# Kernel optimization log

Hardware: AMD Instinct MI355X
Metric: run time of the kernel (lower is better)

Reference implementation:

```python
import jax, jax.numpy as jnp
import numpy as np

K = 1.0      # Lorentz curvature param (geoopt convention: <x,x>_L = -K)
SQK = 1.0    # sqrt(K)
B, LOOKBACK, SEG, D = 256, 4096, 32, 256
N = LOOKBACK // SEG  # 128 segments


def _mink_inner(x, y):
    # Minkowski inner product, keepdims on last axis
    return -x[..., :1] * y[..., :1] + jnp.sum(x[..., 1:] * y[..., 1:], axis=-1, keepdims=True)


def _expmap0_spatial(v):
    # v: [..., D] spatial tangent at origin -> point on hyperboloid [..., D+1]
    n = jnp.linalg.norm(v, axis=-1, keepdims=True)
    ns = jnp.maximum(n, 1e-9)
    x0 = SQK * jnp.cosh(n / SQK)
    xr = SQK * jnp.sinh(n / SQK) * v / ns
    return jnp.concatenate([x0, xr], axis=-1)


def _projx(x):
    # re-project onto hyperboloid: x0 = sqrt(K + ||x_spatial||^2)
    xr = x[..., 1:]
    x0 = jnp.sqrt(K + jnp.sum(xr * xr, axis=-1, keepdims=True))
    return jnp.concatenate([x0, xr], axis=-1)


def _origin_like(x):
    return jnp.zeros_like(x).at[..., 0].set(SQK)


def _logmap(x, y):
    # log_x(y) on the Lorentz manifold
    alpha = jnp.maximum(-_mink_inner(x, y) / K, 1.0 + 1e-7)
    dist = SQK * jnp.arccosh(alpha)
    u = y - alpha * x  # tangent direction (unnormalized)
    un = jnp.sqrt(jnp.maximum(_mink_inner(u, u), 1e-12))
    return dist * u / un


def _expmap(x, u):
    # exp_x(u) on the Lorentz manifold
    un = jnp.sqrt(jnp.maximum(_mink_inner(u, u), 1e-12))
    theta = un / SQK
    return jnp.cosh(theta) * x + jnp.sinh(theta) * SQK * u / un


def _clip_norm(v, max_norm):
    # euclidean-norm clip (torch.norm semantics in source)
    n = jnp.linalg.norm(v, axis=-1, keepdims=True)
    return v / jnp.maximum(n, 1e-12) * jnp.minimum(n, max_norm)


def _encode(x, W, b):
    # [B, lookback] -> [B, N, D]; dropout is identity at eval
    xs = x.reshape(B, N, SEG)
    return jnp.einsum('bns,ds->bnd', xs, W) + b


def _to_hyperbolic(z, effective_scale):
    # vectorized over all segments (original looped over seg_idx)
    v = z * jnp.tanh(effective_scale)
    n = jnp.maximum(jnp.linalg.norm(v, axis=-1, keepdims=True), 1e-8)
    v = v / n * jnp.minimum(n, 1.5)
    return _projx(_expmap0_spatial(v))


def _lorentz_fusion(pts, w):
    # pts: [4, B, N, D+1], w: [4] softmax weights; weighted Karcher mean
    o = _origin_like(pts[0])
    t0 = _logmap(o, pts)                       # tangents at origin (time comp == 0)
    wt = _clip_norm(jnp.einsum('c,cbnd->bnd', w, t0), 2.0)
    mean = _projx(_expmap0_spatial(wt[..., 1:]))  # geoopt expmap0 uses spatial part
    for _ in range(5):                         # fixed 5 Karcher iterations
        tv = _logmap(mean, pts)                # [4, B, N, D+1]
        wv = _clip_norm(jnp.einsum('c,cbnd->bnd', w, tv), 2.0)
        mean = _projx(_expmap(mean, 0.1 * wv))
    return mean


def setup_inputs() -> dict:
    key = jax.random.key(0)
    ks = jax.random.split(key, 12)
    wscale = 1.0 / np.sqrt(SEG)
    inp = {
        'trend': jax.random.normal(ks[0], (B, LOOKBACK), jnp.float32),
        'seasonal_coarse': jax.random.normal(ks[1], (B, LOOKBACK), jnp.float32),
        'seasonal_fine': jax.random.normal(ks[2], (B, LOOKBACK), jnp.float32),
        'residual': jax.random.normal(ks[3], (B, LOOKBACK), jnp.float32),
        'W_trend': jax.random.normal(ks[4], (D, SEG), jnp.float32) * wscale,
        'b_trend': jnp.zeros((D,), jnp.float32),
        'W_coarse': jax.random.normal(ks[5], (D, SEG), jnp.float32) * wscale,
        'b_coarse': jnp.zeros((D,), jnp.float32),
        'W_fine': jax.random.normal(ks[6], (D, SEG), jnp.float32) * wscale,
        'b_fine': jnp.zeros((D,), jnp.float32),
        'W_residual': jax.random.normal(ks[7], (D, SEG), jnp.float32) * wscale,
        'b_residual': jnp.zeros((D,), jnp.float32),
        'effective_scale': jnp.asarray(0.001, jnp.float32),
        'lorentz_weights': jnp.ones((4,), jnp.float32) * 0.25,
    }
    return inp


def reference(trend, seasonal_coarse, seasonal_fine, residual,
              W_trend, b_trend, W_coarse, b_coarse, W_fine, b_fine,
              W_residual, b_residual, effective_scale, lorentz_weights):
    z_t = _encode(trend, W_trend, b_trend)
    z_c = _encode(seasonal_coarse, W_coarse, b_coarse)
    z_f = _encode(seasonal_fine, W_fine, b_fine)
    z_r = _encode(residual, W_residual, b_residual)
    h_t = _to_hyperbolic(z_t, effective_scale)
    h_c = _to_hyperbolic(z_c, effective_scale)
    h_f = _to_hyperbolic(z_f, effective_scale)
    h_r = _to_hyperbolic(z_r, effective_scale)
    w = jax.nn.softmax(lorentz_weights)
    combined = _lorentz_fusion(jnp.stack([h_t, h_c, h_f, h_r], axis=0), w)
    return (h_t, h_c, h_f, h_r, combined)
```

## Files before the change

kernel.cpp:

```cpp
#include <hip/hip_runtime.h>
#include <math.h>

namespace {

typedef float f4 __attribute__((ext_vector_type(4)));

constexpr int PPW  = 4;
constexpr int WPB  = 4;
constexpr int PPB  = PPW * WPB;
constexpr int NPTS = 256 * 128;
constexpr int GRID = NPTS / PPB;
constexpr int OUTS = 257;
constexpr size_t HOFF = (size_t)NPTS * OUTS;
constexpr int LSTR = 256;

__device__ __forceinline__ float frcp(float x)   { return __builtin_amdgcn_rcpf(x); }
__device__ __forceinline__ float fsqrt_(float x) { return __builtin_amdgcn_sqrtf(x); }
__device__ __forceinline__ float facosh(float a) {
  return __logf(a + fsqrt_(fmaf(a, a, -1.f)));
}
__device__ __forceinline__ void fsinhcosh(float x, float& sh, float& ch) {
  float e = __expf(x), ei = frcp(e);
  sh = 0.5f * (e - ei);
  ch = 0.5f * (e + ei);
}
__device__ __forceinline__ float fsinh(float x) {
  float e = __expf(x);
  return 0.5f * (e - frcp(e));
}
__device__ __forceinline__ float dot4(f4 a, f4 b) {
  return a.x * b.x + a.y * b.y + a.z * b.z + a.w * b.w;
}
__device__ __forceinline__ f4 fma4s(float a, f4 b, f4 c) {
  f4 av = {a, a, a, a};
  return __builtin_elementwise_fma(av, b, c);
}

template <int CTRL>
__device__ __forceinline__ float dpp_add(float x) {
  int t = __builtin_amdgcn_update_dpp(0, __builtin_bit_cast(int, x), CTRL, 0xf, 0xf, true);
  return x + __builtin_bit_cast(float, t);
}

template <int NB>
__device__ __forceinline__ void grp_reduce(float* v) {
#pragma unroll
  for (int i = 0; i < NB; ++i) {
    float t = v[i];
    t = dpp_add<0x128>(t);
    t = dpp_add<0x124>(t);
    t = dpp_add<0x122>(t);
    t = dpp_add<0x121>(t);
    v[i] = t;
  }
}

__global__ __launch_bounds__(256) void splmw_kernel(
    const float* __restrict__ xt, const float* __restrict__ xc,
    const float* __restrict__ xf, const float* __restrict__ xr,
    const float* __restrict__ Wt, const float* __restrict__ bt,
    const float* __restrict__ Wc, const float* __restrict__ bc,
    const float* __restrict__ Wf, const float* __restrict__ bf,
    const float* __restrict__ Wr, const float* __restrict__ br,
    const float* __restrict__ esp, const float* __restrict__ lwp,
    float* __restrict__ out) {
  __shared__ float wlds[32 * LSTR];

  const int tid  = threadIdx.x;
  const int lane = tid & 63;
  const int m    = lane & 15;
  const int grp  = lane >> 4;
  const int wv   = tid >> 6;
  const int pt   = blockIdx.x * PPB + wv * PPW + grp;

  float es2 = __expf(2.f * esp[0]);
  const float ts = (es2 - 1.f) * frcp(es2 + 1.f);
  float l0 = lwp[0], l1 = lwp[1], l2 = lwp[2], l3 = lwp[3];
  float mx = fmaxf(fmaxf(l0, l1), fmaxf(l2, l3));
  float e0 = __expf(l0 - mx), e1 = __expf(l1 - mx);
  float e2 = __expf(l2 - mx), e3 = __expf(l3 - mx);
  float ei = frcp(e0 + e1 + e2 + e3);
  const float wgt[4] = {e0 * ei, e1 * ei, e2 * ei, e3 * ei};

  const float* xsarr[4] = {xt, xc, xf, xr};
  const float* Wsarr[4] = {Wt, Wc, Wf, Wr};
  const float* Bsarr[4] = {bt, bc, bf, br};

  f4    h[4][4];
  float x0s[4];
  float r2s[4];

#pragma unroll
  for (int c = 0; c < 4; ++c) {
    const float* Wp = Wsarr[c];
    f4 wrow[8];
#pragma unroll
    for (int k = 0; k < 8; ++k) wrow[k] = *(const f4*)(Wp + tid * 32 + 4 * k);
    __syncthreads();
#pragma unroll
    for (int k = 0; k < 8; ++k) {
      wlds[(4 * k + 0) * LSTR + tid] = wrow[k].x;
      wlds[(4 * k + 1) * LSTR + tid] = wrow[k].y;
      wlds[(4 * k + 2) * LSTR + tid] = wrow[k].z;
      wlds[(4 * k + 3) * LSTR + tid] = wrow[k].w;
    }
    __syncthreads();

    f4 acc[4];
    const float* bp = Bsarr[c];
#pragma unroll
    for (int j = 0; j < 4; ++j) acc[j] = *(const f4*)(bp + 4 * m + 64 * j);
    const float* xp = xsarr[c] + (size_t)pt * 32;
#pragma unroll
    for (int s4 = 0; s4 < 8; ++s4) {
      f4 xq = *(const f4*)(xp + 4 * s4);
      float xa[4] = {xq.x, xq.y, xq.z, xq.w};
#pragma unroll
      for (int si = 0; si < 4; ++si) {
        const float* wr = &wlds[(4 * s4 + si) * LSTR + 4 * m];
#pragma unroll
        for (int j = 0; j < 4; ++j)
          acc[j] = fma4s(xa[si], *(const f4*)(wr + 64 * j), acc[j]);
      }
    }

    float pa = 0.f;
#pragma unroll
    for (int j = 0; j < 4; ++j) {
      h[c][j] = ts * acc[j];
      pa += dot4(h[c][j], h[c][j]);
    }
    grp_reduce<1>(&pa);
    {
      float n1  = fsqrt_(pa);
      float n1m = fmaxf(n1, 1e-8f);
      float c1  = fminf(n1m, 1.5f) * frcp(n1m);
      float n2  = c1 * n1;
      float nsx = fmaxf(n2, 1e-9f);
      float sh  = fsinh(n2);
      float rn  = frcp(nsx);
      float g   = sh * c1 * rn;
      float sxr = sh * n2 * rn;
      float xx0 = fsqrt_(fmaf(sxr, sxr, 1.f));
#pragma unroll
      for (int j = 0; j < 4; ++j) h[c][j] = g * h[c][j];
      x0s[c] = xx0;
      r2s[c] = g * g * pa;
      float* o = out + (size_t)c * HOFF + (size_t)pt * OUTS;
      if (m == 0) o[0] = xx0;
#pragma unroll
      for (int j = 0; j < 4; ++j) {
        int base = 1 + 4 * m + 64 * j;
        f4 v = h[c][j];
        o[base] = v.x; o[base + 1] = v.y; o[base + 2] = v.z; o[base + 3] = v.w;
      }
    }
  }

  float wt0 = 0.f;
  f4    wtr[4];
#pragma unroll
  for (int j = 0; j < 4; ++j) wtr[j] = (f4){0.f, 0.f, 0.f, 0.f};
#pragma unroll
  for (int c = 0; c < 4; ++c) {
    float y0    = x0s[c];
    float alpha = fmaxf(y0, 1.f + 1e-7f);
    float dist  = facosh(alpha);
    float u0    = y0 - alpha;
    float msq   = r2s[c] - u0 * u0;
    float un    = fsqrt_(fmaxf(msq, 1e-12f));
    float f     = wgt[c] * dist * frcp(un);
    wt0 = fmaf(f, u0, wt0);
#pragma unroll
    for (int j = 0; j < 4; ++j) wtr[j] = fma4s(f, h[c][j], wtr[j]);
  }
  float rrp = 0.f;
#pragma unroll
  for (int j = 0; j < 4; ++j) rrp += dot4(wtr[j], wtr[j]);
  grp_reduce<1>(&rrp);

  f4    mr[4];
  float mrr, m0;
  {
    float rr  = rrp;
    float nrm = fsqrt_(fmaf(wt0, wt0, rr));
    float scl = fminf(nrm, 2.f) * frcp(fmaxf(nrm, 1e-12f));
    float nr  = scl * fsqrt_(rr);
    float nsx = fmaxf(nr, 1e-9f);
    float g   = fsinh(nr) * scl * frcp(nsx);
#pragma unroll
    for (int j = 0; j < 4; ++j) mr[j] = g * wtr[j];
    mrr = g * g * rr;
    m0  = fsqrt_(1.f + mrr);
  }

#pragma unroll 1
  for (int it = 0; it < 5; ++it) {
    float dots[4];
#pragma unroll
    for (int c = 0; c < 4; ++c) {
      float d = 0.f;
#pragma unroll
      for (int j = 0; j < 4; ++j) d += dot4(mr[j], h[c][j]);
      dots[c] = d;
    }
    grp_reduce<4>(dots);

    float wv0 = 0.f;
    f4    wvr[4];
#pragma unroll
    for (int j = 0; j < 4; ++j) wvr[j] = (f4){0.f, 0.f, 0.f, 0.f};
#pragma unroll
    for (int c = 0; c < 4; ++c) {
      float d     = dots[c];
      float y0    = x0s[c];
      float ip    = fmaf(m0, y0, -d);
      float alpha = fmaxf(ip, 1.f + 1e-7f);
      float dist  = facosh(alpha);
      float u0    = fmaf(-alpha, m0, y0);
      float t   = fmaf(alpha, mrr, -2.f * d);
      float s2  = fmaf(alpha, t, r2s[c]);
      float msq = s2 - u0 * u0;
      float un  = fsqrt_(fmaxf(msq, 1e-12f));
      float f   = wgt[c] * dist * frcp(un);
      wv0 = fmaf(f, u0, wv0);
#pragma unroll
      for (int j = 0; j < 4; ++j) {
        f4 diff = fma4s(-alpha, mr[j], h[c][j]);
        wvr[j]  = fma4s(f, diff, wvr[j]);
      }
    }
    float pr[2] = {0.f, 0.f};
#pragma unroll
    for (int j = 0; j < 4; ++j) {
      pr[0] += dot4(wvr[j], wvr[j]);
      pr[1] += dot4(mr[j], wvr[j]);
    }
    grp_reduce<2>(pr);

    {
      float rr2  = pr[0];
      float mwv  = pr[1];
      float nrm2 = fsqrt_(fmaf(wv0, wv0, rr2));
      float sc2  = fminf(nrm2, 2.f) * frcp(fmaxf(nrm2, 1e-12f));
      float tt   = 0.1f * sc2;
      float msqu = tt * tt * (rr2 - wv0 * wv0);
      float un2  = fsqrt_(fmaxf(msqu, 1e-12f));
      float shv, chv;
      fsinhcosh(un2, shv, chv);
      float gg = shv * tt * frcp(un2);
#pragma unroll
      for (int j = 0; j < 4; ++j) mr[j] = fma4s(chv, mr[j], gg * wvr[j]);
      mrr = chv * chv * mrr + 2.f * chv * gg * mwv + gg * gg * rr2;
      m0  = fsqrt_(1.f + mrr);
    }
  }

  {
    float* o = out + 4 * HOFF + (size_t)pt * OUTS;
    if (m == 0) o[0] = m0;
#pragma unroll
    for (int j = 0; j < 4; ++j) {
      int base = 1 + 4 * m + 64 * j;
      f4 v = mr[j];
      o[base] = v.x; o[base + 1] = v.y; o[base + 2] = v.z; o[base + 3] = v.w;
    }
  }
}

}

extern "C" void kernel_launch(void* const* d_in, const int* in_sizes, int n_in,
                              void* d_out, int out_size, void* d_ws, size_t ws_size,
                              hipStream_t stream) {
  (void)in_sizes; (void)n_in; (void)out_size; (void)d_ws; (void)ws_size;
  splmw_kernel<<<GRID, 256, 0, stream>>>(
      (const float*)d_in[0], (const float*)d_in[1], (const float*)d_in[2],
      (const float*)d_in[3], (const float*)d_in[4], (const float*)d_in[5],
      (const float*)d_in[6], (const float*)d_in[7], (const float*)d_in[8],
      (const float*)d_in[9], (const float*)d_in[10], (const float*)d_in[11],
      (const float*)d_in[12], (const float*)d_in[13], (float*)d_out);
}
```

Baseline: 281.3 us.

## Reorganize encoder GEMV so each lane computes four points, transpose via LDS

The encoder matmul is restructured so each lane owns four output columns across all four points of its wave. Each weight f4 read from LDS is then reused for four points instead of one, which cuts LDS read traffic. The accumulators are written to a per-wave LDS scratch buffer (padded stride) and read back in the original per-group layout for the rest of the pipeline. This adds an LDS round trip, more LDS allocation, and relies on a wave barrier for intra-wave ordering.

```diff
diff --git a/kernel.cpp b/kernel.cpp
--- a/kernel.cpp
+++ b/kernel.cpp
@@ -12,7 +12,8 @@
 constexpr int GRID = NPTS / PPB;
 constexpr int OUTS = 257;
 constexpr size_t HOFF = (size_t)NPTS * OUTS;
-constexpr int LSTR = 256;
+constexpr int WSTR = 256;
+constexpr int HSTR = 260;
 
 __device__ __forceinline__ float frcp(float x)   { return __builtin_amdgcn_rcpf(x); }
 __device__ __forceinline__ float fsqrt_(float x) { return __builtin_amdgcn_sqrtf(x); }
@@ -64,14 +65,17 @@
     const float* __restrict__ Wr, const float* __restrict__ br,
     const float* __restrict__ esp, const float* __restrict__ lwp,
     float* __restrict__ out) {
-  __shared__ float wlds[32 * LSTR];
+  __shared__ float wlds[32 * WSTR];
+  __shared__ float hlds[WPB * PPW * HSTR];
 
   const int tid  = threadIdx.x;
   const int lane = tid & 63;
   const int m    = lane & 15;
   const int grp  = lane >> 4;
-  const int wv   = tid >> 6;
-  const int pt   = blockIdx.x * PPB + wv * PPW + grp;
+  const int wv   = __builtin_amdgcn_readfirstlane(tid >> 6);
+  const int pt0  = blockIdx.x * PPB + wv * PPW;
+  const int pt   = pt0 + grp;
+  float* hw = hlds + wv * (PPW * HSTR);
 
   float es2 = __expf(2.f * esp[0]);
   const float ts = (es2 - 1.f) * frcp(es2 + 1.f);
@@ -99,35 +103,47 @@
     __syncthreads();
 #pragma unroll
     for (int k = 0; k < 8; ++k) {
-      wlds[(4 * k + 0) * LSTR + tid] = wrow[k].x;
-      wlds[(4 * k + 1) * LSTR + tid] = wrow[k].y;
-      wlds[(4 * k + 2) * LSTR + tid] = wrow[k].z;
-      wlds[(4 * k + 3) * LSTR + tid] = wrow[k].w;
+      wlds[(4 * k + 0) * WSTR + tid] = wrow[k].x;
+      wlds[(4 * k + 1) * WSTR + tid] = wrow[k].y;
+      wlds[(4 * k + 2) * WSTR + tid] = wrow[k].z;
+      wlds[(4 * k + 3) * WSTR + tid] = wrow[k].w;
     }
     __syncthreads();
 
-    f4 acc[4];
-    const float* bp = Bsarr[c];
-#pragma unroll
-    for (int j = 0; j < 4; ++j) acc[j] = *(const f4*)(bp + 4 * m + 64 * j);
-    const float* xp = xsarr[c] + (size_t)pt * 32;
+    f4 acc[PPW];
+    {
+      f4 bv = ((const f4*)Bsarr[c])[lane];
+#pragma unroll
+      for (int p = 0; p < PPW; ++p) acc[p] = bv;
+    }
+    const float* xp = xsarr[c] + (size_t)pt0 * 32;
 #pragma unroll
     for (int s4 = 0; s4 < 8; ++s4) {
-      f4 xq = *(const f4*)(xp + 4 * s4);
-      float xa[4] = {xq.x, xq.y, xq.z, xq.w};
+      f4 q0 = *(const f4*)(xp + 4 * s4);
+      f4 q1 = *(const f4*)(xp + 32 + 4 * s4);
+      f4 q2 = *(const f4*)(xp + 64 + 4 * s4);
+      f4 q3 = *(const f4*)(xp + 96 + 4 * s4);
+      float qa[4][4] = {{q0.x, q0.y, q0.z, q0.w}, {q1.x, q1.y, q1.z, q1.w},
+                        {q2.x, q2.y, q2.z, q2.w}, {q3.x, q3.y, q3.z, q3.w}};
 #pragma unroll
       for (int si = 0; si < 4; ++si) {
-        const float* wr = &wlds[(4 * s4 + si) * LSTR + 4 * m];
-#pragma unroll
-        for (int j = 0; j < 4; ++j)
-          acc[j] = fma4s(xa[si], *(const f4*)(wr + 64 * j), acc[j]);
+        f4 w4 = *(const f4*)&wlds[(4 * s4 + si) * WSTR + 4 * lane];
+#pragma unroll
+        for (int p = 0; p < PPW; ++p) acc[p] = fma4s(qa[p][si], w4, acc[p]);
       }
     }
 
+#pragma unroll
+    for (int p = 0; p < PPW; ++p) *(f4*)&hw[p * HSTR + 4 * lane] = acc[p];
+    __builtin_amdgcn_wave_barrier();
+    f4 zj[4];
+#pragma unroll
+    for (int j = 0; j < 4; ++j) zj[j] = *(const f4*)&hw[grp * HSTR + 4 * m + 64 * j];
+
     float pa = 0.f;
 #pragma unroll
     for (int j = 0; j < 4; ++j) {
-      h[c][j] = ts * acc[j];
+      h[c][j] = ts * zj[j];
       pa += dot4(h[c][j], h[c][j]);
     }
     grp_reduce<1>(&pa);
```

After: 268.8 us. 4.4% less time.

## Split into encode and fusion kernels with per-wave 16-point weight reuse

Applied to the files above, without the earlier changes.

Splits the single fused kernel into two. The encode kernel has each block handle one component, so it loads one weight matrix into LDS once, and each wave computes 16 points with each lane owning 4 output dims, which raises reuse of the weights read from LDS. The fusion kernel then reads the four hyperbolic outputs back from global memory (unaligned 257-stride f4 loads) and recomputes the squared norms. The aim is fewer LDS reloads and barriers per point, at the cost of an extra kernel launch and a full re-read of about 134MB of intermediates.

```diff
diff --git a/kernel.cpp b/kernel.cpp
--- a/kernel.cpp
+++ b/kernel.cpp
@@ -5,14 +5,16 @@
 
 typedef float f4 __attribute__((ext_vector_type(4)));
 
-constexpr int PPW  = 4;
-constexpr int WPB  = 4;
-constexpr int PPB  = PPW * WPB;
 constexpr int NPTS = 256 * 128;
-constexpr int GRID = NPTS / PPB;
 constexpr int OUTS = 257;
 constexpr size_t HOFF = (size_t)NPTS * OUTS;
-constexpr int LSTR = 256;
+
+constexpr int K1_PPW  = 16;
+constexpr int K1_PPB  = 64;
+constexpr int K1_GRID = 4 * (NPTS / K1_PPB);
+
+constexpr int K2_PPB  = 16;
+constexpr int K2_GRID = NPTS / K2_PPB;
 
 __device__ __forceinline__ float frcp(float x)   { return __builtin_amdgcn_rcpf(x); }
 __device__ __forceinline__ float fsqrt_(float x) { return __builtin_amdgcn_sqrtf(x); }
@@ -55,26 +57,114 @@
   }
 }
 
-__global__ __launch_bounds__(256) void splmw_kernel(
+template <int NB>
+__device__ __forceinline__ void wave_reduce64(float* v) {
+  grp_reduce<NB>(v);
+#pragma unroll
+  for (int i = 0; i < NB; ++i) {
+    v[i] += __shfl_xor(v[i], 16, 64);
+    v[i] += __shfl_xor(v[i], 32, 64);
+  }
+}
+
+__global__ __launch_bounds__(256) void encode_kernel(
     const float* __restrict__ xt, const float* __restrict__ xc,
     const float* __restrict__ xf, const float* __restrict__ xr,
     const float* __restrict__ Wt, const float* __restrict__ bt,
     const float* __restrict__ Wc, const float* __restrict__ bc,
     const float* __restrict__ Wf, const float* __restrict__ bf,
     const float* __restrict__ Wr, const float* __restrict__ br,
-    const float* __restrict__ esp, const float* __restrict__ lwp,
-    float* __restrict__ out) {
-  __shared__ float wlds[32 * LSTR];
-
+    const float* __restrict__ esp, float* __restrict__ out) {
+  __shared__ float wlds[32 * 256];
+
+  const int tid  = threadIdx.x;
+  const int lane = tid & 63;
+  const int wv   = __builtin_amdgcn_readfirstlane(tid >> 6);
+  const int bid  = blockIdx.x;
+  const int c    = bid & 3;
+  const int pt0  = (bid >> 2) * K1_PPB + wv * K1_PPW;
+
+  const float* xsarr[4] = {xt, xc, xf, xr};
+  const float* Wsarr[4] = {Wt, Wc, Wf, Wr};
+  const float* Bsarr[4] = {bt, bc, bf, br};
+
+  float es2 = __expf(2.f * esp[0]);
+  const float ts = (es2 - 1.f) * frcp(es2 + 1.f);
+
+  {
+    const float* Wp = Wsarr[c];
+    f4 wrow[8];
+#pragma unroll
+    for (int k = 0; k < 8; ++k) wrow[k] = *(const f4*)(Wp + tid * 32 + 4 * k);
+#pragma unroll
+    for (int k = 0; k < 8; ++k) {
+      wlds[(4 * k + 0) * 256 + tid] = wrow[k].x;
+      wlds[(4 * k + 1) * 256 + tid] = wrow[k].y;
+      wlds[(4 * k + 2) * 256 + tid] = wrow[k].z;
+      wlds[(4 * k + 3) * 256 + tid] = wrow[k].w;
+    }
+  }
+  __syncthreads();
+
+  f4 acc[K1_PPW];
+  {
+    f4 bv = ((const f4*)Bsarr[c])[lane];
+#pragma unroll
+    for (int p = 0; p < K1_PPW; ++p) acc[p] = bv;
+  }
+  const float* xp = xsarr[c] + (size_t)pt0 * 32;
+#pragma unroll
+  for (int s4 = 0; s4 < 8; ++s4) {
+    f4 w4[4];
+#pragma unroll
+    for (int si = 0; si < 4; ++si)
+      w4[si] = *(const f4*)&wlds[(4 * s4 + si) * 256 + 4 * lane];
+#pragma unroll
+    for (int p = 0; p < K1_PPW; ++p) {
+      f4 xq = *(const f4*)(xp + 32 * p + 4 * s4);
+      acc[p] = fma4s(xq.x, w4[0], acc[p]);
+      acc[p] = fma4s(xq.y, w4[1], acc[p]);
+      acc[p] = fma4s(xq.z, w4[2], acc[p]);
+      acc[p] = fma4s(xq.w, w4[3], acc[p]);
+    }
+  }
+
+  float pa[K1_PPW];
+#pragma unroll
+  for (int p = 0; p < K1_PPW; ++p) {
+    acc[p] = ts * acc[p];
+    pa[p]  = dot4(acc[p], acc[p]);
+  }
+  wave_reduce64<K1_PPW>(pa);
+#pragma unroll
+  for (int p = 0; p < K1_PPW; ++p) {
+    float n1  = fsqrt_(pa[p]);
+    float n1m = fmaxf(n1, 1e-8f);
+    float c1  = fminf(n1m, 1.5f) * frcp(n1m);
+    float n2  = c1 * n1;
+    float nsx = fmaxf(n2, 1e-9f);
+    float sh  = fsinh(n2);
+    float rn  = frcp(nsx);
+    float g   = sh * c1 * rn;
+    float sxr = sh * n2 * rn;
+    float xx0 = fsqrt_(fmaf(sxr, sxr, 1.f));
+    f4 v = g * acc[p];
+    float* o = out + (size_t)c * HOFF + (size_t)(pt0 + p) * OUTS;
+    if (lane == 0) o[0] = xx0;
+    int base = 1 + 4 * lane;
+    o[base] = v.x; o[base + 1] = v.y; o[base + 2] = v.z; o[base + 3] = v.w;
+  }
+}
+
+__global__ __launch_bounds__(256) void fusion_kernel(
+    const float* __restrict__ lwp, float* __restrict__ out) {
   const int tid  = threadIdx.x;
   const int lane = tid & 63;
   const int m    = lane & 15;
   const int grp  = lane >> 4;
   const int wv   = tid >> 6;
-  const int pt   = blockIdx.x * PPB + wv * PPW + grp;
-
-  float es2 = __expf(2.f * esp[0]);
-  const float ts = (es2 - 1.f) * frcp(es2 + 1.f);
+  const int pt   = blockIdx.x * K2_PPB + wv * 4 + grp;
+
   float l0 = lwp[0], l1 = lwp[1], l2 = lwp[2], l3 = lwp[3];
   float mx = fmaxf(fmaxf(l0, l1), fmaxf(l2, l3));
   float e0 = __expf(l0 - mx), e1 = __expf(l1 - mx);
@@ -82,79 +172,28 @@
   float ei = frcp(e0 + e1 + e2 + e3);
   const float wgt[4] = {e0 * ei, e1 * ei, e2 * ei, e3 * ei};
 
-  const float* xsarr[4] = {xt, xc, xf, xr};
-  const float* Wsarr[4] = {Wt, Wc, Wf, Wr};
-  const float* Bsarr[4] = {bt, bc, bf, br};
-
   f4    h[4][4];
   float x0s[4];
   float r2s[4];
-
 #pragma unroll
   for (int c = 0; c < 4; ++c) {
-    const float* Wp = Wsarr[c];
-    f4 wrow[8];
-#pragma unroll
-    for (int k = 0; k < 8; ++k) wrow[k] = *(const f4*)(Wp + tid * 32 + 4 * k);
-    __syncthreads();
-#pragma unroll
-    for (int k = 0; k < 8; ++k) {
-      wlds[(4 * k + 0) * LSTR + tid] = wrow[k].x;
-      wlds[(4 * k + 1) * LSTR + tid] = wrow[k].y;
-      wlds[(4 * k + 2) * LSTR + tid] = wrow[k].z;
-      wlds[(4 * k + 3) * LSTR + tid] = wrow[k].w;
-    }
-    __syncthreads();
-
-    f4 acc[4];
-    const float* bp = Bsarr[c];
-#pragma unroll
-    for (int j = 0; j < 4; ++j) acc[j] = *(const f4*)(bp + 4 * m + 64 * j);
-    const float* xp = xsarr[c] + (size_t)pt * 32;
-#pragma unroll
-    for (int s4 = 0; s4 < 8; ++s4) {
-      f4 xq = *(const f4*)(xp + 4 * s4);
-      float xa[4] = {xq.x, xq.y, xq.z, xq.w};
-#pragma unroll
-      for (int si = 0; si < 4; ++si) {
-        const float* wr = &wlds[(4 * s4 + si) * LSTR + 4 * m];
-#pragma unroll
-        for (int j = 0; j < 4; ++j)
-          acc[j] = fma4s(xa[si], *(const f4*)(wr + 64 * j), acc[j]);
-      }
-    }
-
-    float pa = 0.f;
-#pragma unroll
-    for (int j = 0; j < 4; ++j) {
-      h[c][j] = ts * acc[j];
-      pa += dot4(h[c][j], h[c][j]);
-    }
-    grp_reduce<1>(&pa);
-    {
-      float n1  = fsqrt_(pa);
-      float n1m = fmaxf(n1, 1e-8f);
-      float c1  = fminf(n1m, 1.5f) * frcp(n1m);
-      float n2  = c1 * n1;
-      float nsx = fmaxf(n2, 1e-9f);
-      float sh  = fsinh(n2);
-      float rn  = frcp(nsx);
-      float g   = sh * c1 * rn;
-      float sxr = sh * n2 * rn;
-      float xx0 = fsqrt_(fmaf(sxr, sxr, 1.f));
-#pragma unroll
-      for (int j = 0; j < 4; ++j) h[c][j] = g * h[c][j];
-      x0s[c] = xx0;
-      r2s[c] = g * g * pa;
-      float* o = out + (size_t)c * HOFF + (size_t)pt * OUTS;
-      if (m == 0) o[0] = xx0;
-#pragma unroll
-      for (int j = 0; j < 4; ++j) {
-        int base = 1 + 4 * m + 64 * j;
-        f4 v = h[c][j];
-        o[base] = v.x; o[base + 1] = v.y; o[base + 2] = v.z; o[base + 3] = v.w;
-      }
-    }
+    const float* o = out + (size_t)c * HOFF + (size_t)pt * OUTS;
+    x0s[c] = o[0];
+#pragma unroll
+    for (int j = 0; j < 4; ++j) h[c][j] = *(const f4*)&o[1 + 4 * m + 64 * j];
+  }
+  {
+    float pa[4];
+#pragma unroll
+    for (int c = 0; c < 4; ++c) {
+      float s = 0.f;
+#pragma unroll
+      for (int j = 0; j < 4; ++j) s += dot4(h[c][j], h[c][j]);
+      pa[c] = s;
+    }
+    grp_reduce<4>(pa);
+#pragma unroll
+    for (int c = 0; c < 4; ++c) r2s[c] = pa[c];
   }
 
   float wt0 = 0.f;
@@ -274,10 +313,12 @@
                               void* d_out, int out_size, void* d_ws, size_t ws_size,
                               hipStream_t stream) {
   (void)in_sizes; (void)n_in; (void)out_size; (void)d_ws; (void)ws_size;
-  splmw_kernel<<<GRID, 256, 0, stream>>>(
+  encode_kernel<<<K1_GRID, 256, 0, stream>>>(
       (const float*)d_in[0], (const float*)d_in[1], (const float*)d_in[2],
       (const float*)d_in[3], (const float*)d_in[4], (const float*)d_in[5],
       (const float*)d_in[6], (const float*)d_in[7], (const float*)d_in[8],
       (const float*)d_in[9], (const float*)d_in[10], (const float*)d_in[11],
-      (const float*)d_in[12], (const float*)d_in[13], (float*)d_out);
-}
+      (const float*)d_in[12], (float*)d_out);
+  fusion_kernel<<<K2_GRID, 256, 0, stream>>>(
+      (const float*)d_in[13], (float*)d_out);
+}
```

Result: no change. 281.4 us (+0.0%).
